# Optimization experiments

Hardware: AMD Instinct MI355X
Metric: run time of the kernel (lower is better)

The kernel has to match this reference:

```python
import jax, jax.numpy as jnp
import numpy as np

BATCH, C_IN, T, V = 32, 192, 256, 21
HEADS, C_OUT = 3, 192
NEG_SLOPE = 0.2


def setup_inputs() -> dict:
    key = jax.random.key(0)
    k1, k2, k3, k4, k5 = jax.random.split(key, 5)
    x = jax.random.normal(k1, (BATCH, C_IN, T, V), dtype=jnp.float32)
    # adjacency: 0/1 entries, diagonal forced to 1 so every softmax row is valid
    A = (jax.random.uniform(k2, (HEADS, V, V)) > 0.5).astype(jnp.float32)
    d = jnp.arange(V)
    A = A.at[:, d, d].set(1.0)
    W_proj = jax.random.normal(k3, (HEADS * C_OUT, C_IN), dtype=jnp.float32) * 0.05
    score_src = jax.random.normal(k4, (1, HEADS, C_OUT), dtype=jnp.float32) * 0.1
    score_tgt = jax.random.normal(k5, (1, HEADS, C_OUT), dtype=jnp.float32) * 0.1
    return {"x": x, "A": A, "W_proj": W_proj, "score_src": score_src, "score_tgt": score_tgt}


def reference(x, A, W_proj, score_src, score_tgt):
    batch, c_in, t, v = x.shape  # v == 21
    # (b, c, t, v) -> (b, t, v, c); dropout is identity in eval mode
    xp = jnp.transpose(x, (0, 2, 3, 1))
    # linear projection (no bias): (N, heads, C)
    proj = (xp.reshape(-1, c_in) @ W_proj.T).reshape(-1, HEADS, C_OUT)
    N = proj.shape[0]
    Bp = N // v  # = batch * t
    # additive attention scores, reduced over feature dim
    ss = jnp.sum(proj * score_src, axis=-1, keepdims=True)  # (N, H, 1)
    st = jnp.sum(proj * score_tgt, axis=-1, keepdims=True)  # (N, H, 1)
    ss = ss.reshape(Bp, v, HEADS, 1).transpose(0, 2, 1, 3)  # (Bp, H, V, 1)
    st = st.reshape(Bp, v, HEADS, 1).transpose(0, 2, 3, 1)  # (Bp, H, 1, V)
    scores = jax.nn.leaky_relu(ss + st, negative_slope=NEG_SLOPE)  # (Bp, H, V, V)
    # mask zero adjacency entries with -inf, then masked softmax over neighbors
    A_masked = jnp.where(A == 0.0, -jnp.inf, A)  # (H, V, V)
    attn = jax.nn.softmax(scores + A_masked, axis=-1)  # (Bp, H, V, V)
    # aggregate neighbor features per head
    nf = proj.reshape(Bp, v, HEADS, C_OUT).transpose(0, 2, 1, 3)  # (Bp, H, V, C)
    out = jnp.einsum('bhij,bhjc->bhic', attn, nf)  # (Bp, H, V, C)
    # faithful to torch: flatten (Bp*H*V, C) then regroup consecutive triples
    out = out.reshape(-1, 3, C_OUT)  # (N, 3, C)
    # skip connection (last dims always equal) then mean over dim 1
    out = out + proj
    out = out.mean(axis=1)  # (N, C)
    # faithful to torch: raw view back to (batch, C, t, v) (reinterpret, not transpose)
    out = out.reshape(batch, C_OUT, t, v)
    return out
```

## Files before the change

### kernel.cpp

```cpp
#include <hip/hip_runtime.h>
#include <stdint.h>

#define BATCH 32
#define C_IN 192
#define T_DIM 256
#define V_N 21
#define HEADS 3
#define C_OUTD 192
#define NPROJ 576
#define NEG_SLOPE 0.2f
#define W_ELEMS (NPROJ * C_IN)
#define WF_BLOCKS 432

typedef __attribute__((ext_vector_type(8))) short short8;
typedef __attribute__((ext_vector_type(4))) float f32x4;

#define XS_LD 200
#define PROJB_LD 600
#define PROJB_BYTES (21 * PROJB_LD * 2)
#define ATTN2_OFF 25216
#define ATTN2_LD 40
#define SS_OFF (ATTN2_OFF + HEADS * 16 * ATTN2_LD * 2)
#define LDS_TOTAL (SS_OFF + 512)

__device__ __forceinline__ unsigned short f2bf(float f) {
    uint32_t u = __float_as_uint(f);
    u += 0x7fffu + ((u >> 16) & 1u);
    return (unsigned short)(u >> 16);
}
__device__ __forceinline__ float bf2f(unsigned short h) {
    return __uint_as_float(((uint32_t)h) << 16);
}

__global__ void convert_kernel(const float* __restrict__ W,
                               const float* __restrict__ ssrc,
                               const float* __restrict__ stgt,
                               unsigned short* __restrict__ Wf) {
    if (blockIdx.x < WF_BLOCKS) {
        int o = blockIdx.x * 256 + threadIdx.x;
        int j    = o & 7;
        int lane = (o >> 3) & 63;
        int p    = o >> 9;
        int ks   = p % 6;
        int nt   = p / 6;
        int n = nt * 16 + (lane & 15);
        int k = ks * 32 + (lane >> 4) * 8 + j;
        Wf[o] = f2bf(W[n * C_IN + k]);
    } else {
        int h = blockIdx.x - WF_BLOCKS;
        int k = threadIdx.x;
        if (k < C_IN) {
            float ws = 0.f, wt = 0.f;
#pragma unroll 4
            for (int co = 0; co < C_OUTD; co++) {
                float w = W[(h * C_OUTD + co) * C_IN + k];
                ws += w * ssrc[h * C_OUTD + co];
                wt += w * stgt[h * C_OUTD + co];
            }
            int ks = k >> 5;
            int r  = (k >> 3) & 3;
            int j  = k & 7;
            Wf[(((36 * 6 + ks) * 64) + r * 16 + h) * 8 + j]     = f2bf(ws);
            Wf[(((36 * 6 + ks) * 64) + r * 16 + 3 + h) * 8 + j] = f2bf(wt);
        }
    }
}

__global__ __launch_bounds__(512)
void gat_fused_kernel(const float* __restrict__ x,
                      const float* __restrict__ A,
                      const unsigned short* __restrict__ Wf,
                      float* __restrict__ out) {
    __shared__ __align__(16) char lds[LDS_TOTAL];
    unsigned short* xs    = (unsigned short*)lds;
    unsigned short* projb = (unsigned short*)lds;
    unsigned short* attn2 = (unsigned short*)(lds + ATTN2_OFF);
    float* ssl = (float*)(lds + SS_OFF);
    float* stl = (float*)(lds + SS_OFF + 256);

    const int tid  = threadIdx.x;
    const int wv   = tid >> 6;
    const int lane = tid & 63;
    const int q    = lane >> 4;
    const int l15  = lane & 15;
    const int wn   = wv & 3;
    const int wm   = wv >> 2;
    const int bp   = blockIdx.x;
    const int b    = bp >> 8;
    const int t    = bp & 255;

    const float* xb = x + (size_t)b * (C_IN * T_DIM * V_N) + (size_t)t * V_N;
    if (tid < 504) {
        int c0 = tid / 21;
        int v  = tid - c0 * 21;
        const float* p = xb + (size_t)c0 * (T_DIM * V_N) + v;
        float xr[8];
#pragma unroll
        for (int k = 0; k < 8; k++) xr[k] = p[(size_t)k * (24 * T_DIM * V_N)];
        unsigned short* xrow = xs + v * XS_LD + c0;
#pragma unroll
        for (int k = 0; k < 8; k++) xrow[24 * k] = f2bf(xr[k]);
    }
    __syncthreads();

    f32x4 acc[9];
#pragma unroll
    for (int nt = 0; nt < 9; nt++) acc[nt] = (f32x4){0.f, 0.f, 0.f, 0.f};

    const int colbase = wn * 144 + l15;
    const int arow = (wm * 16 + l15) * XS_LD;
    const unsigned short* wf0 = Wf + ((size_t)(wn * 9) * 6) * 512 + lane * 8;
#pragma unroll
    for (int ks = 0; ks < 6; ks++) {
        const int koff = ks * 32 + q * 8;
        short8 a = *(const short8*)(xs + arow + koff);
#pragma unroll
        for (int nt = 0; nt < 9; nt++) {
            short8 bfr = *(const short8*)(wf0 + (nt * 6 + ks) * 512);
            acc[nt] = __builtin_amdgcn_mfma_f32_16x16x32_bf16(a, bfr, acc[nt], 0, 0, 0);
        }
    }

    if (wv == 3 || wv == 7) {
        f32x4 as = (f32x4){0.f, 0.f, 0.f, 0.f};
        const unsigned short* wfs = Wf + (size_t)(36 * 6) * 512 + lane * 8;
#pragma unroll
        for (int ks = 0; ks < 6; ks++) {
            short8 a = *(const short8*)(xs + arow + ks * 32 + q * 8);
            short8 bs = *(const short8*)(wfs + ks * 512);
            as = __builtin_amdgcn_mfma_f32_16x16x32_bf16(a, bs, as, 0, 0, 0);
        }
        if (l15 < 6) {
            float* dst = (l15 < 3) ? ssl : stl;
            int h = (l15 < 3) ? l15 : l15 - 3;
#pragma unroll
            for (int r = 0; r < 4; r++) {
                int v0 = wm * 16 + q * 4 + r;
                if (v0 < 21) dst[v0 * 3 + h] = as[r];
            }
        }
    }
    __syncthreads();

#pragma unroll
    for (int nt = 0; nt < 9; nt++) {
        const int col = colbase + nt * 16;
#pragma unroll
        for (int r = 0; r < 4; r++) {
            int row = wm * 16 + q * 4 + r;
            if (row < 21) projb[row * PROJB_LD + col] = f2bf(acc[nt][r]);
        }
    }

    if (wv < 3 && lane < 21) {
        const int h = wv, i = lane;
        const float* Ah = A + (h * 21 + i) * 21;
        float si = ssl[i * 3 + h];
        float vals[21];
        float mx = -1e30f;
#pragma unroll
        for (int j = 0; j < 21; j++) {
            float a = Ah[j];
            float z = si + stl[j * 3 + h];
            float e = (z > 0.f) ? z : NEG_SLOPE * z;
            float val = (a != 0.f) ? (e + a) : -1e30f;
            vals[j] = val;
            mx = fmaxf(mx, val);
        }
        float sum = 0.f;
#pragma unroll
        for (int j = 0; j < 21; j++) {
            float e = __expf(vals[j] - mx);
            vals[j] = e;
            sum += e;
        }
        float inv = 1.f / sum;
        int m = i / 3;
        bool wr = (i == m * 3);
        unsigned short* drow = attn2 + (h * 16 + m) * ATTN2_LD;
#pragma unroll
        for (int j = 0; j < 21; j++) {
            float vv = vals[j] * inv;
            float s = vv + __shfl_down(vv, 1) + __shfl_down(vv, 2);
            if (wr) drow[j] = f2bf(s);
        }
        if (wr) {
#pragma unroll
            for (int j = 21; j < 32; j++) drow[j] = 0;
        }
    }
    __syncthreads();

    float* outb = out + (size_t)bp * (V_N * C_OUTD);
    int rw[8];
#pragma unroll
    for (int j = 0; j < 8; j++) {
        int row = q * 8 + j;
        rw[j] = ((row > 20) ? 20 : row) * PROJB_LD;
    }
#pragma unroll
    for (int i = 0; i < 5; i++) {
        int p = wv + 8 * i;
        if (p < 36) {
            int h = p / 12;
            int nt = p - h * 12;
            int colh = nt * 16 + l15;
            int col = h * C_OUTD + colh;
            short8 bfr;
#pragma unroll
            for (int j = 0; j < 8; j++) bfr[j] = (short)projb[rw[j] + col];
            short8 av = *(const short8*)(attn2 + (h * 16 + l15) * ATTN2_LD + q * 8);
            f32x4 z = (f32x4){0.f, 0.f, 0.f, 0.f};
            f32x4 d = __builtin_amdgcn_mfma_f32_16x16x32_bf16(av, bfr, z, 0, 0, 0);
#pragma unroll
            for (int r = 0; r < 4; r++) {
                int m = q * 4 + r;
                if (m < 7) {
                    int k = h * 7 + m;
                    float skip = bf2f(projb[k * PROJB_LD + colh])
                               + bf2f(projb[k * PROJB_LD + C_OUTD + colh])
                               + bf2f(projb[k * PROJB_LD + 2 * C_OUTD + colh]);
                    outb[k * C_OUTD + colh] = (d[r] + skip) * (1.f / 3.f);
                }
            }
        }
    }
}

extern "C" void kernel_launch(void* const* d_in, const int* in_sizes, int n_in,
                              void* d_out, int out_size, void* d_ws, size_t ws_size,
                              hipStream_t stream) {
    (void)in_sizes; (void)n_in; (void)out_size; (void)ws_size;
    const float* x    = (const float*)d_in[0];
    const float* A    = (const float*)d_in[1];
    const float* W    = (const float*)d_in[2];
    const float* ssrc = (const float*)d_in[3];
    const float* stgt = (const float*)d_in[4];
    float* out = (float*)d_out;
    unsigned short* Wf = (unsigned short*)d_ws;

    convert_kernel<<<WF_BLOCKS + HEADS, 256, 0, stream>>>(W, ssrc, stgt, Wf);
    gat_fused_kernel<<<BATCH * T_DIM, 512, 0, stream>>>(x, A, Wf, out);
}
```

Before: 466.8 us.

## Halve block size to four waves, each computing both row tiles

The fused GAT kernel now runs with 256 threads per block instead of 512. Each wave does the projection MFMA twice: once for rows 16-20 and once for rows 0-15. The x staging, score computation and aggregation loops are rebalanced across the four waves. This is meant to cut per-block thread overhead and let each wave do more work, but LDS use per block is unchanged, so fewer resident waves per CU are available to hide latency.

```diff
diff --git a/kernel.cpp b/kernel.cpp
--- a/kernel.cpp
+++ b/kernel.cpp
@@ -66,7 +66,7 @@
     }
 }
 
-__global__ __launch_bounds__(512)
+__global__ __launch_bounds__(256)
 void gat_fused_kernel(const float* __restrict__ x,
                       const float* __restrict__ A,
                       const unsigned short* __restrict__ Wf,
@@ -83,60 +83,105 @@
     const int lane = tid & 63;
     const int q    = lane >> 4;
     const int l15  = lane & 15;
-    const int wn   = wv & 3;
-    const int wm   = wv >> 2;
     const int bp   = blockIdx.x;
     const int b    = bp >> 8;
     const int t    = bp & 255;
 
     const float* xb = x + (size_t)b * (C_IN * T_DIM * V_N) + (size_t)t * V_N;
-    if (tid < 504) {
+    if (tid < 252) {
         int c0 = tid / 21;
         int v  = tid - c0 * 21;
         const float* p = xb + (size_t)c0 * (T_DIM * V_N) + v;
+        unsigned short* xrow = xs + v * XS_LD + c0;
         float xr[8];
 #pragma unroll
-        for (int k = 0; k < 8; k++) xr[k] = p[(size_t)k * (24 * T_DIM * V_N)];
-        unsigned short* xrow = xs + v * XS_LD + c0;
-#pragma unroll
-        for (int k = 0; k < 8; k++) xrow[24 * k] = f2bf(xr[k]);
+        for (int k = 0; k < 8; k++) xr[k] = p[(size_t)k * (12 * T_DIM * V_N)];
+#pragma unroll
+        for (int k = 0; k < 8; k++) xrow[12 * k] = f2bf(xr[k]);
+#pragma unroll
+        for (int k = 8; k < 16; k++) xr[k - 8] = p[(size_t)k * (12 * T_DIM * V_N)];
+#pragma unroll
+        for (int k = 8; k < 16; k++) xrow[12 * k] = f2bf(xr[k - 8]);
     }
     __syncthreads();
 
+    const int colbase = wv * 144 + l15;
+    const unsigned short* wf0 = Wf + ((size_t)(wv * 9) * 6) * 512 + lane * 8;
+    const unsigned short* wfs = Wf + (size_t)(36 * 6) * 512 + lane * 8;
+
     f32x4 acc[9];
+
 #pragma unroll
     for (int nt = 0; nt < 9; nt++) acc[nt] = (f32x4){0.f, 0.f, 0.f, 0.f};
-
-    const int colbase = wn * 144 + l15;
-    const int arow = (wm * 16 + l15) * XS_LD;
-    const unsigned short* wf0 = Wf + ((size_t)(wn * 9) * 6) * 512 + lane * 8;
-#pragma unroll
-    for (int ks = 0; ks < 6; ks++) {
-        const int koff = ks * 32 + q * 8;
-        short8 a = *(const short8*)(xs + arow + koff);
-#pragma unroll
-        for (int nt = 0; nt < 9; nt++) {
-            short8 bfr = *(const short8*)(wf0 + (nt * 6 + ks) * 512);
-            acc[nt] = __builtin_amdgcn_mfma_f32_16x16x32_bf16(a, bfr, acc[nt], 0, 0, 0);
-        }
-    }
-
-    if (wv == 3 || wv == 7) {
-        f32x4 as = (f32x4){0.f, 0.f, 0.f, 0.f};
-        const unsigned short* wfs = Wf + (size_t)(36 * 6) * 512 + lane * 8;
+    {
+        const int arow = (16 + l15) * XS_LD;
 #pragma unroll
         for (int ks = 0; ks < 6; ks++) {
             short8 a = *(const short8*)(xs + arow + ks * 32 + q * 8);
-            short8 bs = *(const short8*)(wfs + ks * 512);
-            as = __builtin_amdgcn_mfma_f32_16x16x32_bf16(a, bs, as, 0, 0, 0);
-        }
-        if (l15 < 6) {
-            float* dst = (l15 < 3) ? ssl : stl;
-            int h = (l15 < 3) ? l15 : l15 - 3;
+#pragma unroll
+            for (int nt = 0; nt < 9; nt++) {
+                short8 bfr = *(const short8*)(wf0 + (nt * 6 + ks) * 512);
+                acc[nt] = __builtin_amdgcn_mfma_f32_16x16x32_bf16(a, bfr, acc[nt], 0, 0, 0);
+            }
+        }
+        if (wv == 3) {
+            f32x4 as = (f32x4){0.f, 0.f, 0.f, 0.f};
+#pragma unroll
+            for (int ks = 0; ks < 6; ks++) {
+                short8 a = *(const short8*)(xs + arow + ks * 32 + q * 8);
+                short8 bs = *(const short8*)(wfs + ks * 512);
+                as = __builtin_amdgcn_mfma_f32_16x16x32_bf16(a, bs, as, 0, 0, 0);
+            }
+            if (l15 < 6) {
+                float* dst = (l15 < 3) ? ssl : stl;
+                int h = (l15 < 3) ? l15 : l15 - 3;
+#pragma unroll
+                for (int r = 0; r < 4; r++) {
+                    int v1 = 16 + q * 4 + r;
+                    if (v1 < 21) dst[v1 * 3 + h] = as[r];
+                }
+            }
+        }
+#pragma unroll
+        for (int nt = 0; nt < 9; nt++) {
+            const int col = colbase + nt * 16;
 #pragma unroll
             for (int r = 0; r < 4; r++) {
-                int v0 = wm * 16 + q * 4 + r;
-                if (v0 < 21) dst[v0 * 3 + h] = as[r];
+                int row = 16 + q * 4 + r;
+                if (row < 21) projb[row * PROJB_LD + col] = f2bf(acc[nt][r]);
+            }
+        }
+    }
+
+#pragma unroll
+    for (int nt = 0; nt < 9; nt++) acc[nt] = (f32x4){0.f, 0.f, 0.f, 0.f};
+    {
+        const int arow = l15 * XS_LD;
+#pragma unroll
+        for (int ks = 0; ks < 6; ks++) {
+            short8 a = *(const short8*)(xs + arow + ks * 32 + q * 8);
+#pragma unroll
+            for (int nt = 0; nt < 9; nt++) {
+                short8 bfr = *(const short8*)(wf0 + (nt * 6 + ks) * 512);
+                acc[nt] = __builtin_amdgcn_mfma_f32_16x16x32_bf16(a, bfr, acc[nt], 0, 0, 0);
+            }
+        }
+        if (wv == 3) {
+            f32x4 as = (f32x4){0.f, 0.f, 0.f, 0.f};
+#pragma unroll
+            for (int ks = 0; ks < 6; ks++) {
+                short8 a = *(const short8*)(xs + arow + ks * 32 + q * 8);
+                short8 bs = *(const short8*)(wfs + ks * 512);
+                as = __builtin_amdgcn_mfma_f32_16x16x32_bf16(a, bs, as, 0, 0, 0);
+            }
+            if (l15 < 6) {
+                float* dst = (l15 < 3) ? ssl : stl;
+                int h = (l15 < 3) ? l15 : l15 - 3;
+#pragma unroll
+                for (int r = 0; r < 4; r++) {
+                    int v0 = q * 4 + r;
+                    dst[v0 * 3 + h] = as[r];
+                }
             }
         }
     }
@@ -147,8 +192,8 @@
         const int col = colbase + nt * 16;
 #pragma unroll
         for (int r = 0; r < 4; r++) {
-            int row = wm * 16 + q * 4 + r;
-            if (row < 21) projb[row * PROJB_LD + col] = f2bf(acc[nt][r]);
+            int row = q * 4 + r;
+            projb[row * PROJB_LD + col] = f2bf(acc[nt][r]);
         }
     }
 
@@ -199,29 +244,27 @@
         rw[j] = ((row > 20) ? 20 : row) * PROJB_LD;
     }
 #pragma unroll
-    for (int i = 0; i < 5; i++) {
-        int p = wv + 8 * i;
-        if (p < 36) {
-            int h = p / 12;
-            int nt = p - h * 12;
-            int colh = nt * 16 + l15;
-            int col = h * C_OUTD + colh;
-            short8 bfr;
-#pragma unroll
-            for (int j = 0; j < 8; j++) bfr[j] = (short)projb[rw[j] + col];
-            short8 av = *(const short8*)(attn2 + (h * 16 + l15) * ATTN2_LD + q * 8);
-            f32x4 z = (f32x4){0.f, 0.f, 0.f, 0.f};
-            f32x4 d = __builtin_amdgcn_mfma_f32_16x16x32_bf16(av, bfr, z, 0, 0, 0);
-#pragma unroll
-            for (int r = 0; r < 4; r++) {
-                int m = q * 4 + r;
-                if (m < 7) {
-                    int k = h * 7 + m;
-                    float skip = bf2f(projb[k * PROJB_LD + colh])
-                               + bf2f(projb[k * PROJB_LD + C_OUTD + colh])
-                               + bf2f(projb[k * PROJB_LD + 2 * C_OUTD + colh]);
-                    outb[k * C_OUTD + colh] = (d[r] + skip) * (1.f / 3.f);
-                }
+    for (int i = 0; i < 9; i++) {
+        int p = wv * 9 + i;
+        int h = p / 12;
+        int nt = p - h * 12;
+        int colh = nt * 16 + l15;
+        int col = h * C_OUTD + colh;
+        short8 bfr;
+#pragma unroll
+        for (int j = 0; j < 8; j++) bfr[j] = (short)projb[rw[j] + col];
+        short8 av = *(const short8*)(attn2 + (h * 16 + l15) * ATTN2_LD + q * 8);
+        f32x4 z = (f32x4){0.f, 0.f, 0.f, 0.f};
+        f32x4 d = __builtin_amdgcn_mfma_f32_16x16x32_bf16(av, bfr, z, 0, 0, 0);
+#pragma unroll
+        for (int r = 0; r < 4; r++) {
+            int m = q * 4 + r;
+            if (m < 7) {
+                int k = h * 7 + m;
+                float skip = bf2f(projb[k * PROJB_LD + colh])
+                           + bf2f(projb[k * PROJB_LD + C_OUTD + colh])
+                           + bf2f(projb[k * PROJB_LD + 2 * C_OUTD + colh]);
+                outb[k * C_OUTD + colh] = (d[r] + skip) * (1.f / 3.f);
             }
         }
     }
@@ -240,5 +283,5 @@
     unsigned short* Wf = (unsigned short*)d_ws;
 
     convert_kernel<<<WF_BLOCKS + HEADS, 256, 0, stream>>>(W, ssrc, stgt, Wf);
-    gat_fused_kernel<<<BATCH * T_DIM, 512, 0, stream>>>(x, A, Wf, out);
-}
+    gat_fused_kernel<<<BATCH * T_DIM, 256, 0, stream>>>(x, A, Wf, out);
+}
```

New measurement: 448.4 us. 1.04x faster.
